# Performance work log

Hardware: AMD Instinct MI355X
Metric: run time of the kernel (lower is better)

## Reference

```python
import jax, jax.numpy as jnp
import numpy as np
import math

SENTINEL = 1.0e6  # eta/phi value assigned to inactive (pt<=0) objects
BIG = 1.0e6       # dR placeholder for non-lower-triangular entries


def _remove_duplicates(objs, threshold):
    """objs: (B, n, 3) with columns (pt, eta, phi). Zeros out objects that
    are within dR < threshold of a later object in the group (faithful to
    the TF strictly-lower-triangular / reduce over rows logic)."""
    n = objs.shape[1]
    active = objs[..., 0] > 0.0                              # (B, n)
    eta = jnp.where(active, objs[..., 1], SENTINEL)
    phi = jnp.where(active, objs[..., 2], SENTINEL)
    deta = eta[:, :, None] - eta[:, None, :]                 # (B, n, n)
    dphi = jnp.mod(phi[:, :, None] - phi[:, None, :] + math.pi,
                   2.0 * math.pi) - math.pi
    dr2 = deta * deta + dphi * dphi
    # strictly lower triangular mask (row i > col j), same as
    # logical_not(band_part(ones, 0, -1)) in TF
    tri = jnp.tril(jnp.ones((n, n), dtype=bool), k=-1)       # (n, n)
    # safe sqrt: only evaluate where the mask keeps the value
    dr = jnp.sqrt(jnp.where(tri, dr2, 1.0))
    replaced = jnp.where(tri, dr, BIG)                       # (B, n, n)
    # TF reduce_any(..., axis=0) per event -> axis=1 of batched tensor
    duplicates = jnp.any(replaced < threshold, axis=1)       # (B, n)
    return jnp.where(duplicates[..., None], 0.0, objs)


def duplicate_removal(x, threshold):
    jets = _remove_duplicates(x[:, 0:6], threshold)
    electrons = _remove_duplicates(x[:, 6:9], threshold)
    muons = _remove_duplicates(x[:, 9:12], threshold)
    photons = _remove_duplicates(x[:, 12:15], threshold)
    met = x[:, 15:16]
    return jnp.concatenate([jets, electrons, muons, photons, met], axis=1)


def setup_inputs() -> dict:
    key = jax.random.key(0)
    x = jax.random.normal(key, (1000000, 16, 3), dtype=jnp.float32)
    return {"x": x}


def reference(x):
    return duplicate_removal(x, 0.05)
```

## Files before the change

kernel.cpp:

```cpp
#include <hip/hip_runtime.h>
#include <math.h>

#define PI_F        3.14159274101257324e0f
#define TWOPI_F     6.28318548202514648e0f
#define INV_TWOPI_F (1.0f / TWOPI_F)

#define DR2_LT      0.0025f

#define ROWS_PER_BLOCK 128
#define ROW_STRIDE     49

__device__ __forceinline__ int pair_close(float ei, float ej, float pi_, float pj) {
    float deta = __fsub_rn(ei, ej);
    float dd   = __fadd_rn(__fsub_rn(pi_, pj), PI_F);
    float q    = truncf(__fmul_rn(dd, INV_TWOPI_F));
    float m    = __fmaf_rn(q, -TWOPI_F, dd);
    if (m < 0.0f) m = __fadd_rn(m, TWOPI_F);
    float dphi = __fsub_rn(m, PI_F);
    float dr2  = __fadd_rn(__fmul_rn(deta, deta), __fmul_rn(dphi, dphi));
    return dr2 < DR2_LT;
}

__device__ __forceinline__ float lds_at(const float* r, int u) {
    return r[12 * (u & 3) + (u >> 2)];
}

template <int OFF, int N>
__device__ __forceinline__ unsigned group_dup(const float* r) {
    float e[N], p[N];
    int   a[N];
#pragma unroll
    for (int k = 0; k < N; ++k) {
        int u = 3 * (OFF + k);
        a[k] = lds_at(r, u + 0) > 0.0f;
        e[k] = lds_at(r, u + 1);
        p[k] = lds_at(r, u + 2);
    }
    unsigned dup = 0;
#pragma unroll
    for (int j = 0; j < N - 1; ++j) {
        int d = 0;
#pragma unroll
        for (int i = j + 1; i < N; ++i) {
            int close = pair_close(e[i], e[j], p[i], p[j]);
            d |= (a[i] & a[j] & close) | ((a[i] | a[j]) ^ 1);
        }
        if (d) dup |= (1u << (OFF + j));
    }
    return dup;
}

template <bool FULL>
__device__ __forceinline__ void block_body(
    const float4* __restrict__ in, float4* __restrict__ out, int B,
    float* rowbuf, unsigned long long* maskbuf) {
    const int t = threadIdx.x;
    const long long base4  = (long long)blockIdx.x * (ROWS_PER_BLOCK * 12);
    const long long total4 = (long long)B * 12;

    float4 v[6];
#pragma unroll
    for (int i = 0; i < 6; ++i) {
        long long g = base4 + t + 256 * i;
        if (FULL || g < total4) {
            v[i] = in[g];
            int local = t + 256 * i;
            int rl = local / 12;
            int f  = local - rl * 12;
            float* dstp = &rowbuf[rl * ROW_STRIDE + f];
            dstp[0] = v[i].x; dstp[12] = v[i].y; dstp[24] = v[i].z; dstp[36] = v[i].w;
        }
    }
    __syncthreads();

    if (t < ROWS_PER_BLOCK) {
        int row = blockIdx.x * ROWS_PER_BLOCK + t;
        unsigned dup = 0;
        if (FULL || row < B) {
            const float* r = rowbuf + t * ROW_STRIDE;
            dup  = group_dup<0, 6>(r);
            dup |= group_dup<6, 3>(r);
            dup |= group_dup<9, 3>(r);
            dup |= group_dup<12, 3>(r);
        }
        unsigned long long fm = 0ull;
#pragma unroll
        for (int o = 0; o < 15; ++o)
            fm |= (unsigned long long)((dup >> o) & 1u) * (7ull << (3 * o));
        maskbuf[t] = fm;
    }
    __syncthreads();

#pragma unroll
    for (int i = 0; i < 6; ++i) {
        long long g = base4 + t + 256 * i;
        if (FULL || g < total4) {
            int local = t + 256 * i;
            int rl = local / 12;
            int f  = local - rl * 12;
            unsigned nib = (unsigned)(maskbuf[rl] >> (4 * f)) & 0xFu;
            float4 w = v[i];
            if (nib & 1u) w.x = 0.0f;
            if (nib & 2u) w.y = 0.0f;
            if (nib & 4u) w.z = 0.0f;
            if (nib & 8u) w.w = 0.0f;
            out[g] = w;
        }
    }
}

__global__ __launch_bounds__(256, 4) void dup_removal_kernel(
    const float4* __restrict__ in, float4* __restrict__ out, int B) {
    __shared__ float rowbuf[ROWS_PER_BLOCK * ROW_STRIDE];
    __shared__ unsigned long long maskbuf[ROWS_PER_BLOCK];

    const long long base4  = (long long)blockIdx.x * (ROWS_PER_BLOCK * 12);
    const long long total4 = (long long)B * 12;
    if (base4 + ROWS_PER_BLOCK * 12 <= total4)
        block_body<true>(in, out, B, rowbuf, maskbuf);
    else
        block_body<false>(in, out, B, rowbuf, maskbuf);
}

extern "C" void kernel_launch(void* const* d_in, const int* in_sizes, int n_in,
                              void* d_out, int out_size, void* d_ws, size_t ws_size,
                              hipStream_t stream) {
    const float4* x = (const float4*)d_in[0];
    float4* out = (float4*)d_out;
    int B = in_sizes[0] / 48;
    int grid = (B + ROWS_PER_BLOCK - 1) / ROWS_PER_BLOCK;
    dup_removal_kernel<<<grid, 256, 0, stream>>>(x, out, B);
}
```

Before: 318.3 us.

## Halve rows per block, reread tile from LDS, raise occupancy bound

Cuts rows per block from 128 to 64, so each thread loads 3 float4s instead of 6. Input values are no longer kept in registers across the compute phase; the masked output is rebuilt from the LDS tile. Launch bounds go from 4 to 8 waves-per-EU hint, 64-bit index math becomes 32-bit, and LDS per block shrinks. The aim is more resident blocks to hide memory latency. The cost is that only 64 of 256 threads run the pairwise compute, and the extra LDS reads.

```diff
diff --git a/kernel.cpp b/kernel.cpp
--- a/kernel.cpp
+++ b/kernel.cpp
@@ -7,7 +7,8 @@
 
 #define DR2_LT      0.0025f
 
-#define ROWS_PER_BLOCK 128
+#define ROWS_PER_BLOCK 64
+#define THREADS        256
 #define ROW_STRIDE     49
 
 __device__ __forceinline__ int pair_close(float ei, float ej, float pi_, float pj) {
@@ -55,20 +56,19 @@
     const float4* __restrict__ in, float4* __restrict__ out, int B,
     float* rowbuf, unsigned long long* maskbuf) {
     const int t = threadIdx.x;
-    const long long base4  = (long long)blockIdx.x * (ROWS_PER_BLOCK * 12);
-    const long long total4 = (long long)B * 12;
+    const int base4  = blockIdx.x * (ROWS_PER_BLOCK * 12);
+    const int total4 = B * 12;
 
-    float4 v[6];
 #pragma unroll
-    for (int i = 0; i < 6; ++i) {
-        long long g = base4 + t + 256 * i;
+    for (int i = 0; i < 3; ++i) {
+        int g = base4 + t + THREADS * i;
         if (FULL || g < total4) {
-            v[i] = in[g];
-            int local = t + 256 * i;
+            float4 v = in[g];
+            int local = t + THREADS * i;
             int rl = local / 12;
             int f  = local - rl * 12;
             float* dstp = &rowbuf[rl * ROW_STRIDE + f];
-            dstp[0] = v[i].x; dstp[12] = v[i].y; dstp[24] = v[i].z; dstp[36] = v[i].w;
+            dstp[0] = v.x; dstp[12] = v.y; dstp[24] = v.z; dstp[36] = v.w;
         }
     }
     __syncthreads();
@@ -92,30 +92,31 @@
     __syncthreads();
 
 #pragma unroll
-    for (int i = 0; i < 6; ++i) {
-        long long g = base4 + t + 256 * i;
+    for (int i = 0; i < 3; ++i) {
+        int g = base4 + t + THREADS * i;
         if (FULL || g < total4) {
-            int local = t + 256 * i;
+            int local = t + THREADS * i;
             int rl = local / 12;
             int f  = local - rl * 12;
             unsigned nib = (unsigned)(maskbuf[rl] >> (4 * f)) & 0xFu;
-            float4 w = v[i];
-            if (nib & 1u) w.x = 0.0f;
-            if (nib & 2u) w.y = 0.0f;
-            if (nib & 4u) w.z = 0.0f;
-            if (nib & 8u) w.w = 0.0f;
+            const float* srcp = &rowbuf[rl * ROW_STRIDE + f];
+            float4 w;
+            w.x = (nib & 1u) ? 0.0f : srcp[0];
+            w.y = (nib & 2u) ? 0.0f : srcp[12];
+            w.z = (nib & 4u) ? 0.0f : srcp[24];
+            w.w = (nib & 8u) ? 0.0f : srcp[36];
             out[g] = w;
         }
     }
 }
 
-__global__ __launch_bounds__(256, 4) void dup_removal_kernel(
+__global__ __launch_bounds__(THREADS, 8) void dup_removal_kernel(
     const float4* __restrict__ in, float4* __restrict__ out, int B) {
     __shared__ float rowbuf[ROWS_PER_BLOCK * ROW_STRIDE];
     __shared__ unsigned long long maskbuf[ROWS_PER_BLOCK];
 
-    const long long base4  = (long long)blockIdx.x * (ROWS_PER_BLOCK * 12);
-    const long long total4 = (long long)B * 12;
+    const int base4  = blockIdx.x * (ROWS_PER_BLOCK * 12);
+    const int total4 = B * 12;
     if (base4 + ROWS_PER_BLOCK * 12 <= total4)
         block_body<true>(in, out, B, rowbuf, maskbuf);
     else
@@ -129,5 +130,5 @@
     float4* out = (float4*)d_out;
     int B = in_sizes[0] / 48;
     int grid = (B + ROWS_PER_BLOCK - 1) / ROWS_PER_BLOCK;
-    dup_removal_kernel<<<grid, 256, 0, stream>>>(x, out, B);
+    dup_removal_kernel<<<grid, THREADS, 0, stream>>>(x, out, B);
 }
```

After: 318.4 us. Within noise of the previous version (+0.0%).
